# Kernel tuning notes

Measured on AMD Instinct MI355X. Metric: run time of the kernel, lower is better.

The kernel has to match this reference:

```python
import jax, jax.numpy as jnp
import numpy as np

N = 100000
E = 1600000
H = 128
M = 256
L = 6
G = 512          # number of graphs in the batch
A = 95           # num_atom_types
EXTRA = 3        # input_dim - 1
EPS = 1e-5


def swish(x):
    return x * jax.nn.sigmoid(x)


def setup_inputs() -> dict:
    key = jax.random.key(0)
    ks = jax.random.split(key, 16)
    z = jax.random.randint(ks[0], (N, 1), 0, A).astype(jnp.float32)
    extra = jax.random.normal(ks[1], (N, EXTRA), dtype=jnp.float32)
    x = jnp.concatenate([z, extra], axis=1)                     # [N, 4]
    edge_index = jax.random.randint(ks[2], (2, E), 0, N)        # [2, E]
    batch = jnp.sort(jax.random.randint(ks[3], (N,), 0, G))     # [N]
    s = 0.02
    z_embed = jax.random.normal(ks[4], (A, H), dtype=jnp.float32) * s
    extra_w = jax.random.normal(ks[5], (H, EXTRA), dtype=jnp.float32) * (1.0 / np.sqrt(EXTRA))
    extra_b = jnp.zeros((H,), jnp.float32)
    conv_w = jax.random.normal(ks[6], (L, H, H), dtype=jnp.float32) * (1.0 / np.sqrt(H))
    conv_b = jnp.zeros((L, H), jnp.float32)
    gamma = jnp.ones((L, H), jnp.float32)
    beta = jnp.zeros((L, H), jnp.float32)
    mean_scale = jnp.ones((L, H), jnp.float32)
    mlp_w1 = jax.random.normal(ks[7], (L, M, H), dtype=jnp.float32) * (1.0 / np.sqrt(H))
    mlp_b1 = jnp.zeros((L, M), jnp.float32)
    mlp_w2 = jax.random.normal(ks[8], (L, H, M), dtype=jnp.float32) * (1.0 / np.sqrt(M))
    mlp_b2 = jnp.zeros((L, H), jnp.float32)
    return dict(x=x, edge_index=edge_index, batch=batch, z_embed=z_embed,
                extra_w=extra_w, extra_b=extra_b, conv_w=conv_w, conv_b=conv_b,
                gamma=gamma, beta=beta, mean_scale=mean_scale,
                mlp_w1=mlp_w1, mlp_b1=mlp_b1, mlp_w2=mlp_w2, mlp_b2=mlp_b2)


def gnn_forward(x, edge_index, batch, z_embed, extra_w, extra_b, conv_w, conv_b,
                gamma, beta, mean_scale, mlp_w1, mlp_b1, mlp_w2, mlp_b2):
    z = x[:, 0].astype(jnp.int32)
    h = z_embed[z] + x[:, 1:] @ extra_w.T + extra_b                 # [N, H]

    # GCN: add self loops, symmetric normalization (computed once; graph is static)
    loop = jnp.arange(N)
    src = jnp.concatenate([edge_index[0], loop])
    dst = jnp.concatenate([edge_index[1], loop])
    deg = jax.ops.segment_sum(jnp.ones_like(dst, jnp.float32), dst, num_segments=N)
    dinv = jnp.where(deg > 0, jax.lax.rsqrt(jnp.maximum(deg, 1.0)), 0.0)
    norm = (dinv[src] * dinv[dst])[:, None]                         # [E+N, 1]

    cnt = jax.ops.segment_sum(jnp.ones((N,), jnp.float32), batch, num_segments=G)[:, None]
    cnt = jnp.maximum(cnt, 1.0)

    for i in range(L):
        h_res = h
        # GCNConv
        xw = h @ conv_w[i].T
        agg = jax.ops.segment_sum(xw[src] * norm, dst, num_segments=N) + conv_b[i]
        # GraphNorm: gamma * (x - alpha*mean) / sqrt(var + eps) + beta, per graph
        mean = jax.ops.segment_sum(agg, batch, num_segments=G) / cnt   # [G, H]
        sub = agg - mean_scale[i] * mean[batch]
        var = jax.ops.segment_sum(sub * sub, batch, num_segments=G) / cnt
        hn = gamma[i] * sub * jax.lax.rsqrt(var[batch] + EPS) + beta[i]
        ha = swish(hn)
        # residual MLP
        h = swish(swish(ha @ mlp_w1[i].T + mlp_b1[i]) @ mlp_w2[i].T + mlp_b2[i]) + h_res
    return h


def reference(x, edge_index, batch, z_embed, extra_w, extra_b, conv_w, conv_b,
              gamma, beta, mean_scale, mlp_w1, mlp_b1, mlp_w2, mlp_b2):
    return gnn_forward(x, edge_index, batch, z_embed, extra_w, extra_b, conv_w, conv_b,
                       gamma, beta, mean_scale, mlp_w1, mlp_b1, mlp_w2, mlp_b2)
```

## Files before the change

kernel.cpp:

```cpp
#include <hip/hip_runtime.h>

#define NN 100000
#define EE 1600000
#define HH 128
#define MM 256
#define LL 6
#define GG 512
#define SCAN_NB ((NN + 1023) / 1024)

typedef __attribute__((ext_vector_type(8))) short short8;
typedef __attribute__((ext_vector_type(4))) float floatx4;

__device__ __forceinline__ float swishf(float v) {
    return v / (1.0f + __expf(-v));
}

__device__ __forceinline__ unsigned short f2bf(float f) {
    unsigned u = __builtin_bit_cast(unsigned, f);
    unsigned r = u + 0x7FFFu + ((u >> 16) & 1u);
    return (unsigned short)(r >> 16);
}

__device__ __forceinline__ float bf2f(unsigned short u) {
    return __builtin_bit_cast(float, (unsigned)u << 16);
}

__device__ __forceinline__ float2 bf2f2(unsigned u) {
    float2 r;
    r.x = __builtin_bit_cast(float, u << 16);
    r.y = __builtin_bit_cast(float, u & 0xFFFF0000u);
    return r;
}

__device__ __forceinline__ void unpack8(uint4 v, float* a) {
    float2 p0 = bf2f2(v.x), p1 = bf2f2(v.y), p2 = bf2f2(v.z), p3 = bf2f2(v.w);
    a[0] = p0.x; a[1] = p0.y; a[2] = p1.x; a[3] = p1.y;
    a[4] = p2.x; a[5] = p2.y; a[6] = p3.x; a[7] = p3.y;
}

__device__ __forceinline__ uint4 pack8(const float* o) {
    uint4 pk;
    pk.x = (unsigned)f2bf(o[0]) | ((unsigned)f2bf(o[1]) << 16);
    pk.y = (unsigned)f2bf(o[2]) | ((unsigned)f2bf(o[3]) << 16);
    pk.z = (unsigned)f2bf(o[4]) | ((unsigned)f2bf(o[5]) << 16);
    pk.w = (unsigned)f2bf(o[6]) | ((unsigned)f2bf(o[7]) << 16);
    return pk;
}

__device__ __forceinline__ uint2 pack4(const float* o) {
    uint2 pk;
    pk.x = (unsigned)f2bf(o[0]) | ((unsigned)f2bf(o[1]) << 16);
    pk.y = (unsigned)f2bf(o[2]) | ((unsigned)f2bf(o[3]) << 16);
    return pk;
}

__global__ void k_embed(const float* __restrict__ x, const float* __restrict__ z_embed,
                        const float* __restrict__ ew, const float* __restrict__ eb,
                        unsigned short* __restrict__ hb) {
    int idx = blockIdx.x * blockDim.x + threadIdx.x;
    if (idx >= NN * 32) return;
    int n = idx >> 5;
    int c0 = (idx & 31) << 2;
    const float* xr = x + (size_t)n * 4;
    int z = (int)xr[0];
    float x1 = xr[1], x2 = xr[2], x3 = xr[3];
    const float* ze = z_embed + (size_t)z * HH + c0;
    float o[4];
#pragma unroll
    for (int j = 0; j < 4; ++j) {
        int c = c0 + j;
        o[j] = ze[j] + x1 * ew[c * 3 + 0] + x2 * ew[c * 3 + 1] + x3 * ew[c * 3 + 2] + eb[c];
    }
    *(uint2*)(hb + (size_t)n * HH + c0) = pack4(o);
}

__global__ void k_f2bf3(const float* __restrict__ s1, unsigned short* __restrict__ d1, int n1,
                        const float* __restrict__ s2, unsigned short* __restrict__ d2, int n2,
                        const float* __restrict__ s3, unsigned short* __restrict__ d3, int n3) {
    int i = blockIdx.x * blockDim.x + threadIdx.x;
    if (i < n1) {
        d1[i] = f2bf(s1[i]);
    } else if (i < n1 + n2) {
        d2[i - n1] = f2bf(s2[i - n1]);
    } else if (i < n1 + n2 + n3) {
        d3[i - n1 - n2] = f2bf(s3[i - n1 - n2]);
    }
}

__global__ __launch_bounds__(256) void k_degree_p(const int* __restrict__ dst,
                                                  int* __restrict__ deg) {
    int part = blockIdx.x & 7;
    int blk = blockIdx.x >> 3;
    int nb = gridDim.x >> 3;
    int lo = (int)((long long)part * NN / 8);
    int hi = (int)((long long)(part + 1) * NN / 8);
    for (int e = blk * 256 + threadIdx.x; e < EE; e += nb * 256) {
        int d = dst[e];
        if (d >= lo && d < hi) atomicAdd(&deg[d], 1);
    }
}

__global__ void k_dinv(const int* __restrict__ deg, float* __restrict__ dinv) {
    int n = blockIdx.x * blockDim.x + threadIdx.x;
    if (n < NN) dinv[n] = rsqrtf((float)(deg[n] + 1));
}

__global__ void k_scan1(const int* __restrict__ deg, int* __restrict__ bsum) {
    __shared__ int sd[256];
    int t = threadIdx.x;
    int base = blockIdx.x * 1024 + t * 4;
    int s = 0;
#pragma unroll
    for (int j = 0; j < 4; ++j) {
        int i = base + j;
        if (i < NN) s += deg[i];
    }
    sd[t] = s;
    __syncthreads();
    for (int off = 128; off > 0; off >>= 1) {
        if (t < off) sd[t] += sd[t + off];
        __syncthreads();
    }
    if (t == 0) bsum[blockIdx.x] = sd[0];
}

__global__ void k_scan2(const int* __restrict__ bsum, int* __restrict__ boff) {
    __shared__ int sd[128];
    int t = threadIdx.x;
    int v = (t < SCAN_NB) ? bsum[t] : 0;
    sd[t] = v;
    __syncthreads();
    for (int off = 1; off < 128; off <<= 1) {
        int u = (t >= off) ? sd[t - off] : 0;
        __syncthreads();
        sd[t] += u;
        __syncthreads();
    }
    boff[t] = sd[t] - v;
}

__global__ void k_scan3(const int* __restrict__ deg, const int* __restrict__ boff,
                        int* __restrict__ rowptr) {
    __shared__ int sd[256];
    int t = threadIdx.x;
    int base = blockIdx.x * 1024 + t * 4;
    int v[4];
    int s = 0;
#pragma unroll
    for (int j = 0; j < 4; ++j) {
        int i = base + j;
        v[j] = (i < NN) ? deg[i] : 0;
        s += v[j];
    }
    sd[t] = s;
    __syncthreads();
    for (int off = 1; off < 256; off <<= 1) {
        int u = (t >= off) ? sd[t - off] : 0;
        __syncthreads();
        sd[t] += u;
        __syncthreads();
    }
    int run = boff[blockIdx.x] + sd[t] - s;
#pragma unroll
    for (int j = 0; j < 4; ++j) {
        int i = base + j;
        if (i < NN) rowptr[i] = run;
        if (i == NN - 1) rowptr[NN] = run + v[j];
        run += v[j];
    }
}

__global__ __launch_bounds__(256) void k_fill_p(const int* __restrict__ ei,
                                                const int* __restrict__ rowptr,
                                                int* __restrict__ cursor,
                                                int* __restrict__ col) {
    int part = blockIdx.x & 7;
    int blk = blockIdx.x >> 3;
    int nb = gridDim.x >> 3;
    int lo = (int)((long long)part * NN / 8);
    int hi = (int)((long long)(part + 1) * NN / 8);
    for (int e = blk * 256 + threadIdx.x; e < EE; e += nb * 256) {
        int d = ei[EE + e];
        if (d >= lo && d < hi) {
            int p = atomicAdd(&cursor[d], 1);
            col[rowptr[d] + p] = ei[e];
        }
    }
}

__global__ void k_gptr(const int* __restrict__ batch, int* __restrict__ gptr) {
    int n = blockIdx.x * blockDim.x + threadIdx.x;
    if (n >= NN) return;
    int b = batch[n];
    int pb = (n == 0) ? -1 : batch[n - 1];
    for (int g = pb + 1; g <= b; ++g) gptr[g] = n;
    if (n == NN - 1) {
        for (int g = b + 1; g <= GG; ++g) gptr[g] = NN;
    }
}

__global__ __launch_bounds__(256) void k_conv(const unsigned short* __restrict__ A,
                                              const unsigned short* __restrict__ B,
                                              const float* __restrict__ dinv,
                                              unsigned short* __restrict__ Cb) {
    __shared__ unsigned short Bs[128][HH + 8];
    const int tid = threadIdx.x;
    const int wave = tid >> 6;
    const int lane = tid & 63;
    const int quad = lane >> 4;
    const int l16 = lane & 15;
    const int wr = (wave & 1) << 6;
    const int wc = (wave >> 1) << 6;
    const int rowBase = blockIdx.x * 128;

    for (int i = tid; i < 128 * (HH / 8); i += 256) {
        int r = i / (HH / 8);
        int kk = (i % (HH / 8)) * 8;
        int rho = (r & 64) | ((r & 3) << 4) | ((r >> 2) & 15);
        *(uint4*)(&Bs[rho][kk]) = *(const uint4*)(B + (size_t)r * HH + kk);
    }

    floatx4 acc[4][4];
    const floatx4 zed = {0.f, 0.f, 0.f, 0.f};
#pragma unroll
    for (int i = 0; i < 4; ++i)
#pragma unroll
        for (int j = 0; j < 4; ++j) acc[i][j] = zed;

    int ar[4];
#pragma unroll
    for (int i = 0; i < 4; ++i) {
        int r = rowBase + wr + (i << 4) + l16;
        ar[i] = r < NN ? r : NN - 1;
    }

    __syncthreads();

#pragma unroll
    for (int ks = 0; ks < HH / 32; ++ks) {
        int k = (ks << 5) + (quad << 3);
        short8 a[4], b[4];
#pragma unroll
        for (int i = 0; i < 4; ++i) a[i] = *(const short8*)(A + (size_t)ar[i] * HH + k);
#pragma unroll
        for (int j = 0; j < 4; ++j) b[j] = *(const short8*)(&Bs[wc + (j << 4) + l16][k]);
#pragma unroll
        for (int i = 0; i < 4; ++i)
#pragma unroll
            for (int j = 0; j < 4; ++j)
                acc[i][j] =
                    __builtin_amdgcn_mfma_f32_16x16x32_bf16(a[i], b[j], acc[i][j], 0, 0, 0);
    }

    const int c0 = wc + (l16 << 2);
#pragma unroll
    for (int i = 0; i < 4; ++i) {
        int rb = rowBase + wr + (i << 4) + (quad << 2);
#pragma unroll
        for (int reg = 0; reg < 4; ++reg) {
            int r = rb + reg;
            if (r < NN) {
                float dv = dinv[r];
                float o[4];
#pragma unroll
                for (int j = 0; j < 4; ++j) o[j] = acc[i][j][reg] * dv;
                *(uint2*)(Cb + (size_t)r * HH + c0) = pack4(o);
            }
        }
    }
}

__global__ __launch_bounds__(256) void k_agg(const unsigned short* __restrict__ y,
                                             const int* __restrict__ rowptr,
                                             const int* __restrict__ col,
                                             const float* __restrict__ dinv,
                                             const float* __restrict__ cb,
                                             unsigned short* __restrict__ agg) {
    int w = threadIdx.x >> 6;
    int lane = threadIdx.x & 63;
    int d = blockIdx.x * 4 + w;
    if (d >= NN) return;
    int grp = lane >> 4;
    int l16 = lane & 15;
    const uint4* yv = (const uint4*)y;
    float acc[8];
#pragma unroll
    for (int j = 0; j < 8; ++j) acc[j] = 0.f;
    if (grp == 0) {
        uint4 v = yv[(size_t)d * 16 + l16];
        unpack8(v, acc);
    }
    int beg = rowptr[d];
    int end = rowptr[d + 1];
    for (int e = beg + grp; e < end; e += 4) {
        int s = col[e];
        uint4 v = yv[(size_t)s * 16 + l16];
        float b0[8];
        unpack8(v, b0);
#pragma unroll
        for (int k = 0; k < 8; ++k) acc[k] += b0[k];
    }
#pragma unroll
    for (int j = 0; j < 8; ++j) {
        acc[j] += __shfl_xor(acc[j], 16, 64);
        acc[j] += __shfl_xor(acc[j], 32, 64);
    }
    if (grp == 0) {
        float dv = dinv[d];
        float4 c0 = *(const float4*)(cb + l16 * 8);
        float4 c1 = *(const float4*)(cb + l16 * 8 + 4);
        float o[8];
        o[0] = acc[0] * dv + c0.x; o[1] = acc[1] * dv + c0.y;
        o[2] = acc[2] * dv + c0.z; o[3] = acc[3] * dv + c0.w;
        o[4] = acc[4] * dv + c1.x; o[5] = acc[5] * dv + c1.y;
        o[6] = acc[6] * dv + c1.z; o[7] = acc[7] * dv + c1.w;
        *(uint4*)(agg + (size_t)d * HH + l16 * 8) = pack8(o);
    }
}

__global__ __launch_bounds__(512) void k_stats(const unsigned short* __restrict__ agg,
                                               const int* __restrict__ gptr,
                                               const float* __restrict__ ms,
                                               const float* __restrict__ gamma,
                                               const float* __restrict__ beta,
                                               float* __restrict__ c1,
                                               float* __restrict__ c0) {
    __shared__ float s1[512];
    __shared__ float s2[512];
    int g = blockIdx.x;
    int t = threadIdx.x;
    int c = t & 127;
    int part = t >> 7;
    int beg = gptr[g];
    int end = gptr[g + 1];
    float S1 = 0.f, S2 = 0.f;
    for (int n = beg + part; n < end; n += 4) {
        float v = bf2f(agg[(size_t)n * HH + c]);
        S1 += v;
        S2 += v * v;
    }
    s1[t] = S1;
    s2[t] = S2;
    __syncthreads();
    if (part == 0) {
        S1 = (s1[c] + s1[c + 128]) + (s1[c + 256] + s1[c + 384]);
        S2 = (s2[c] + s2[c + 128]) + (s2[c + 256] + s2[c + 384]);
        int cnt = end - beg;
        float inv = 1.0f / (float)(cnt > 0 ? cnt : 1);
        float m = S1 * inv;
        float msc = ms[c];
        float var = S2 * inv - msc * (2.0f - msc) * m * m;
        float rstd = rsqrtf(var + 1e-5f);
        float c1v = gamma[c] * rstd;
        c1[g * HH + c] = c1v;
        c0[g * HH + c] = beta[c] - c1v * msc * m;
    }
}

__global__ __launch_bounds__(256) void k_mega(const unsigned short* __restrict__ agg,
                                              const int* __restrict__ batch,
                                              const float* __restrict__ c1,
                                              const float* __restrict__ c0,
                                              const unsigned short* __restrict__ W1,
                                              const float* __restrict__ b1,
                                              const unsigned short* __restrict__ W2,
                                              const float* __restrict__ b2,
                                              const unsigned short* __restrict__ Wc,
                                              const float* __restrict__ dinv,
                                              unsigned short* __restrict__ hb,
                                              float* __restrict__ h_out,
                                              unsigned short* __restrict__ y_out, int writeF,
                                              int doConv) {
    __shared__ unsigned short ha_s[64 * 136];
    __shared__ unsigned short ts[64 * 264];
    const int tid = threadIdx.x;
    const int wave = tid >> 6;
    const int lane = tid & 63;
    const int quad = lane >> 4;
    const int l16 = lane & 15;
    const int rowBase = blockIdx.x * 64;
    const floatx4 zed = {0.f, 0.f, 0.f, 0.f};

    {
        int lr = tid >> 2;
        int coff = (tid & 3) << 5;
        int r = rowBase + lr;
        if (r >= NN) r = NN - 1;
        int g = batch[r];
        const float* c1p = c1 + g * HH + coff;
        const float* c0p = c0 + g * HH + coff;
#pragma unroll
        for (int q = 0; q < 4; ++q) {
            uint4 raw = *(const uint4*)(agg + (size_t)r * HH + coff + (q << 3));
            float v[8];
            unpack8(raw, v);
            float4 ca = *(const float4*)(c1p + (q << 3));
            float4 cb4 = *(const float4*)(c1p + (q << 3) + 4);
            float4 da = *(const float4*)(c0p + (q << 3));
            float4 db = *(const float4*)(c0p + (q << 3) + 4);
            float cc1[8] = {ca.x, ca.y, ca.z, ca.w, cb4.x, cb4.y, cb4.z, cb4.w};
            float cc0[8] = {da.x, da.y, da.z, da.w, db.x, db.y, db.z, db.w};
            float o[8];
#pragma unroll
            for (int j = 0; j < 8; ++j) o[j] = swishf(cc1[j] * v[j] + cc0[j]);
            *(uint4*)(&ha_s[lr * 136 + coff + (q << 3)]) = pack8(o);
        }
    }
    __syncthreads();

    {
        const int wca = wave << 6;
        floatx4 acc1[4][4];
#pragma unroll
        for (int i = 0; i < 4; ++i)
#pragma unroll
            for (int j = 0; j < 4; ++j) acc1[i][j] = zed;
#pragma unroll
        for (int ks = 0; ks < 4; ++ks) {
            int k = (ks << 5) + (quad << 3);
            short8 a[4], b[4];
#pragma unroll
            for (int i = 0; i < 4; ++i)
                a[i] = *(const short8*)(&ha_s[((i << 4) + l16) * 136 + k]);
#pragma unroll
            for (int j = 0; j < 4; ++j)
                b[j] = *(const short8*)(W1 + (size_t)(wca + (l16 << 2) + j) * HH + k);
#pragma unroll
            for (int i = 0; i < 4; ++i)
#pragma unroll
                for (int j = 0; j < 4; ++j)
                    acc1[i][j] =
                        __builtin_amdgcn_mfma_f32_16x16x32_bf16(a[i], b[j], acc1[i][j], 0, 0, 0);
        }
        const int ct = wca + (l16 << 2);
        float4 b4 = *(const float4*)(b1 + ct);
        float bv[4] = {b4.x, b4.y, b4.z, b4.w};
#pragma unroll
        for (int i = 0; i < 4; ++i) {
#pragma unroll
            for (int reg = 0; reg < 4; ++reg) {
                int lr = (i << 4) + (quad << 2) + reg;
                float o[4];
#pragma unroll
                for (int j = 0; j < 4; ++j) o[j] = swishf(acc1[i][j][reg] + bv[j]);
                *(uint2*)(&ts[lr * 264 + ct]) = pack4(o);
            }
        }
    }
    __syncthreads();

    const int wrb = (wave & 1) << 5;
    const int wcb = (wave >> 1) << 6;
    const int co = wcb + (l16 << 2);
    {
        floatx4 acc2[2][4];
#pragma unroll
        for (int i = 0; i < 2; ++i)
#pragma unroll
            for (int j = 0; j < 4; ++j) acc2[i][j] = zed;
#pragma unroll
        for (int ks = 0; ks < 8; ++ks) {
            int k = (ks << 5) + (quad << 3);
            short8 a[2], b[4];
#pragma unroll
            for (int i = 0; i < 2; ++i)
                a[i] = *(const short8*)(&ts[(wrb + (i << 4) + l16) * 264 + k]);
#pragma unroll
            for (int j = 0; j < 4; ++j)
                b[j] = *(const short8*)(W2 + (size_t)(wcb + (l16 << 2) + j) * MM + k);
#pragma unroll
            for (int i = 0; i < 2; ++i)
#pragma unroll
                for (int j = 0; j < 4; ++j)
                    acc2[i][j] =
                        __builtin_amdgcn_mfma_f32_16x16x32_bf16(a[i], b[j], acc2[i][j], 0, 0, 0);
        }
        float4 b4 = *(const float4*)(b2 + co);
        float bv[4] = {b4.x, b4.y, b4.z, b4.w};
#pragma unroll
        for (int i = 0; i < 2; ++i) {
#pragma unroll
            for (int reg = 0; reg < 4; ++reg) {
                int lr = wrb + (i << 4) + (quad << 2) + reg;
                int r = rowBase + lr;
                if (r < NN) {
                    uint2 rv = *(const uint2*)(hb + (size_t)r * HH + co);
                    float2 r01 = bf2f2(rv.x), r23 = bf2f2(rv.y);
                    float o[4];
                    o[0] = swishf(acc2[i][0][reg] + bv[0]) + r01.x;
                    o[1] = swishf(acc2[i][1][reg] + bv[1]) + r01.y;
                    o[2] = swishf(acc2[i][2][reg] + bv[2]) + r23.x;
                    o[3] = swishf(acc2[i][3][reg] + bv[3]) + r23.y;
                    uint2 pk = pack4(o);
                    *(uint2*)(hb + (size_t)r * HH + co) = pk;
                    if (writeF)
                        *(float4*)(h_out + (size_t)r * HH + co) =
                            make_float4(o[0], o[1], o[2], o[3]);
                    *(uint2*)(&ha_s[lr * 136 + co]) = pk;
                } else {
                    *(uint2*)(&ha_s[lr * 136 + co]) = make_uint2(0u, 0u);
                }
            }
        }
    }

    if (doConv) {
        __syncthreads();
        floatx4 acc3[2][4];
#pragma unroll
        for (int i = 0; i < 2; ++i)
#pragma unroll
            for (int j = 0; j < 4; ++j) acc3[i][j] = zed;
#pragma unroll
        for (int ks = 0; ks < 4; ++ks) {
            int k = (ks << 5) + (quad << 3);
            short8 a[2], b[4];
#pragma unroll
            for (int i = 0; i < 2; ++i)
                a[i] = *(const short8*)(&ha_s[(wrb + (i << 4) + l16) * 136 + k]);
#pragma unroll
            for (int j = 0; j < 4; ++j)
                b[j] = *(const short8*)(Wc + (size_t)(wcb + (l16 << 2) + j) * HH + k);
#pragma unroll
            for (int i = 0; i < 2; ++i)
#pragma unroll
                for (int j = 0; j < 4; ++j)
                    acc3[i][j] =
                        __builtin_amdgcn_mfma_f32_16x16x32_bf16(a[i], b[j], acc3[i][j], 0, 0, 0);
        }
#pragma unroll
        for (int i = 0; i < 2; ++i) {
#pragma unroll
            for (int reg = 0; reg < 4; ++reg) {
                int r = rowBase + wrb + (i << 4) + (quad << 2) + reg;
                if (r < NN) {
                    float dv = dinv[r];
                    float o[4];
#pragma unroll
                    for (int j = 0; j < 4; ++j) o[j] = acc3[i][j][reg] * dv;
                    *(uint2*)(y_out + (size_t)r * HH + co) = pack4(o);
                }
            }
        }
    }
}

extern "C" void kernel_launch(void* const* d_in, const int* in_sizes, int n_in,
                              void* d_out, int out_size, void* d_ws, size_t ws_size,
                              hipStream_t stream) {
    const float* x = (const float*)d_in[0];
    const int* ei = (const int*)d_in[1];
    const int* batch = (const int*)d_in[2];
    const float* z_embed = (const float*)d_in[3];
    const float* extra_w = (const float*)d_in[4];
    const float* extra_b = (const float*)d_in[5];
    const float* conv_w = (const float*)d_in[6];
    const float* conv_b = (const float*)d_in[7];
    const float* gamma = (const float*)d_in[8];
    const float* beta = (const float*)d_in[9];
    const float* mean_scale = (const float*)d_in[10];
    const float* mlp_w1 = (const float*)d_in[11];
    const float* mlp_b1 = (const float*)d_in[12];
    const float* mlp_w2 = (const float*)d_in[13];
    const float* mlp_b2 = (const float*)d_in[14];
    float* h_out = (float*)d_out;

    char* wsB = (char*)d_ws;
    size_t off = 0;
    auto alloc = [&](size_t bytes) -> void* {
        void* p = (void*)(wsB + off);
        off = (off + bytes + 255) & ~(size_t)255;
        return p;
    };
    float* dinv = (float*)alloc((size_t)NN * 4);
    int* deg = (int*)alloc((size_t)NN * 4);
    int* cursor = (int*)alloc((size_t)NN * 4);
    int* rowptr = (int*)alloc((size_t)(NN + 1) * 4);
    int* bsum = (int*)alloc(128 * 4);
    int* boff = (int*)alloc(128 * 4);
    int* col = (int*)alloc((size_t)EE * 4);
    int* gptr = (int*)alloc((size_t)(GG + 1) * 4);
    float* c1t = (float*)alloc((size_t)GG * HH * 4);
    float* c0t = (float*)alloc((size_t)GG * HH * 4);
    unsigned short* wb =
        (unsigned short*)alloc((size_t)(LL * (HH * HH + MM * HH + HH * MM)) * 2);
    unsigned short* cwb = wb;
    unsigned short* w1b = wb + (size_t)LL * HH * HH;
    unsigned short* w2b = w1b + (size_t)LL * MM * HH;
    unsigned short* hb = (unsigned short*)alloc((size_t)NN * HH * 2);
    unsigned short* ybuf = (unsigned short*)alloc((size_t)NN * HH * 2);
    unsigned short* aggb = (unsigned short*)alloc((size_t)NN * HH * 2);

    hipMemsetAsync(deg, 0, (size_t)NN * 4, stream);
    hipMemsetAsync(cursor, 0, (size_t)NN * 4, stream);

    k_embed<<<(NN * 32 + 255) / 256, 256, 0, stream>>>(x, z_embed, extra_w, extra_b, hb);
    {
        int n1 = LL * HH * HH, n2 = LL * MM * HH, n3 = LL * HH * MM;
        int nt = n1 + n2 + n3;
        k_f2bf3<<<(nt + 255) / 256, 256, 0, stream>>>(conv_w, cwb, n1, mlp_w1, w1b, n2,
                                                      mlp_w2, w2b, n3);
    }
    k_degree_p<<<1024, 256, 0, stream>>>(ei + EE, deg);
    k_dinv<<<(NN + 255) / 256, 256, 0, stream>>>(deg, dinv);
    k_scan1<<<SCAN_NB, 256, 0, stream>>>(deg, bsum);
    k_scan2<<<1, 128, 0, stream>>>(bsum, boff);
    k_scan3<<<SCAN_NB, 256, 0, stream>>>(deg, boff, rowptr);
    k_fill_p<<<1024, 256, 0, stream>>>(ei, rowptr, cursor, col);
    k_gptr<<<(NN + 255) / 256, 256, 0, stream>>>(batch, gptr);

    int gconv = (NN + 127) / 128;
    int gmega = (NN + 63) / 64;
    k_conv<<<gconv, 256, 0, stream>>>(hb, cwb, dinv, ybuf);
    for (int i = 0; i < LL; ++i) {
        k_agg<<<(NN + 3) / 4, 256, 0, stream>>>(ybuf, rowptr, col, dinv,
                                                conv_b + (size_t)i * HH, aggb);
        k_stats<<<GG, 512, 0, stream>>>(aggb, gptr, mean_scale + (size_t)i * HH,
                                        gamma + (size_t)i * HH, beta + (size_t)i * HH, c1t,
                                        c0t);
        k_mega<<<gmega, 256, 0, stream>>>(
            aggb, batch, c1t, c0t, w1b + (size_t)i * MM * HH, mlp_b1 + (size_t)i * MM,
            w2b + (size_t)i * HH * MM, mlp_b2 + (size_t)i * HH,
            cwb + (size_t)(i + 1 < LL ? i + 1 : 0) * HH * HH, dinv, hb, h_out, ybuf,
            i == LL - 1 ? 1 : 0, i < LL - 1 ? 1 : 0);
    }
}
```

Before: 1.346 ms.

## Fuse per-graph GraphNorm statistics into aggregation kernel via atomics

The aggregation kernel now also accumulates per-graph sum and sum-of-squares. It reduces the four rows handled by a block in shared memory and adds them to global buffers with atomics, which removes the separate k_stats pass that re-read the whole agg tensor. A small finalize kernel then turns the sums into the scale and shift coefficients and zeroes the accumulators for the next layer. In exchange it adds a block-wide sync and many float atomics per block, and summation order becomes nondeterministic. k_mega also gains a launch-bounds occupancy hint of 3.

New measurement: 1.334 ms. About the same (-0.9%).

```diff
diff --git a/kernel.cpp b/kernel.cpp
--- a/kernel.cpp
+++ b/kernel.cpp
@@ -275,23 +275,32 @@
                                              const int* __restrict__ col,
                                              const float* __restrict__ dinv,
                                              const float* __restrict__ cb,
-                                             unsigned short* __restrict__ agg) {
+                                             const int* __restrict__ batch,
+                                             unsigned short* __restrict__ agg,
+                                             float* __restrict__ S1g,
+                                             float* __restrict__ S2g) {
+    __shared__ float s1s[4][128];
+    __shared__ float s2s[4][128];
+    __shared__ int sg[4];
     int w = threadIdx.x >> 6;
     int lane = threadIdx.x & 63;
     int d = blockIdx.x * 4 + w;
-    if (d >= NN) return;
+    bool valid = d < NN;
     int grp = lane >> 4;
     int l16 = lane & 15;
     const uint4* yv = (const uint4*)y;
     float acc[8];
 #pragma unroll
     for (int j = 0; j < 8; ++j) acc[j] = 0.f;
-    if (grp == 0) {
+    if (grp == 0 && valid) {
         uint4 v = yv[(size_t)d * 16 + l16];
         unpack8(v, acc);
     }
-    int beg = rowptr[d];
-    int end = rowptr[d + 1];
+    int beg = 0, end = 0;
+    if (valid) {
+        beg = rowptr[d];
+        end = rowptr[d + 1];
+    }
     for (int e = beg + grp; e < end; e += 4) {
         int s = col[e];
         uint4 v = yv[(size_t)s * 16 + l16];
@@ -306,71 +315,100 @@
         acc[j] += __shfl_xor(acc[j], 32, 64);
     }
     if (grp == 0) {
-        float dv = dinv[d];
-        float4 c0 = *(const float4*)(cb + l16 * 8);
-        float4 c1 = *(const float4*)(cb + l16 * 8 + 4);
-        float o[8];
-        o[0] = acc[0] * dv + c0.x; o[1] = acc[1] * dv + c0.y;
-        o[2] = acc[2] * dv + c0.z; o[3] = acc[3] * dv + c0.w;
-        o[4] = acc[4] * dv + c1.x; o[5] = acc[5] * dv + c1.y;
-        o[6] = acc[6] * dv + c1.z; o[7] = acc[7] * dv + c1.w;
-        *(uint4*)(agg + (size_t)d * HH + l16 * 8) = pack8(o);
-    }
-}
-
-__global__ __launch_bounds__(512) void k_stats(const unsigned short* __restrict__ agg,
-                                               const int* __restrict__ gptr,
-                                               const float* __restrict__ ms,
-                                               const float* __restrict__ gamma,
-                                               const float* __restrict__ beta,
-                                               float* __restrict__ c1,
-                                               float* __restrict__ c0) {
-    __shared__ float s1[512];
-    __shared__ float s2[512];
+        if (valid) {
+            float dv = dinv[d];
+            float4 c0 = *(const float4*)(cb + l16 * 8);
+            float4 c1 = *(const float4*)(cb + l16 * 8 + 4);
+            float o[8];
+            o[0] = acc[0] * dv + c0.x; o[1] = acc[1] * dv + c0.y;
+            o[2] = acc[2] * dv + c0.z; o[3] = acc[3] * dv + c0.w;
+            o[4] = acc[4] * dv + c1.x; o[5] = acc[5] * dv + c1.y;
+            o[6] = acc[6] * dv + c1.z; o[7] = acc[7] * dv + c1.w;
+            unsigned short us[8];
+#pragma unroll
+            for (int j = 0; j < 8; ++j) us[j] = f2bf(o[j]);
+            uint4 pk;
+            pk.x = (unsigned)us[0] | ((unsigned)us[1] << 16);
+            pk.y = (unsigned)us[2] | ((unsigned)us[3] << 16);
+            pk.z = (unsigned)us[4] | ((unsigned)us[5] << 16);
+            pk.w = (unsigned)us[6] | ((unsigned)us[7] << 16);
+            *(uint4*)(agg + (size_t)d * HH + l16 * 8) = pk;
+#pragma unroll
+            for (int j = 0; j < 8; ++j) {
+                float orv = bf2f(us[j]);
+                s1s[w][l16 * 8 + j] = orv;
+                s2s[w][l16 * 8 + j] = orv * orv;
+            }
+        } else {
+#pragma unroll
+            for (int j = 0; j < 8; ++j) {
+                s1s[w][l16 * 8 + j] = 0.f;
+                s2s[w][l16 * 8 + j] = 0.f;
+            }
+        }
+        if (l16 == 0) sg[w] = valid ? batch[d] : -1;
+    }
+    __syncthreads();
+    if (threadIdx.x < 128) {
+        int c = threadIdx.x;
+        int g0 = sg[0], g1 = sg[1], g2 = sg[2], g3 = sg[3];
+        if (g0 >= 0 && g0 == g1 && g0 == g2 && g0 == g3) {
+            float a = (s1s[0][c] + s1s[1][c]) + (s1s[2][c] + s1s[3][c]);
+            float b = (s2s[0][c] + s2s[1][c]) + (s2s[2][c] + s2s[3][c]);
+            atomicAdd(&S1g[g0 * HH + c], a);
+            atomicAdd(&S2g[g0 * HH + c], b);
+        } else {
+            int gs[4] = {g0, g1, g2, g3};
+#pragma unroll
+            for (int ww = 0; ww < 4; ++ww) {
+                if (gs[ww] >= 0) {
+                    atomicAdd(&S1g[gs[ww] * HH + c], s1s[ww][c]);
+                    atomicAdd(&S2g[gs[ww] * HH + c], s2s[ww][c]);
+                }
+            }
+        }
+    }
+}
+
+__global__ __launch_bounds__(128) void k_finalize(const int* __restrict__ gptr,
+                                                  const float* __restrict__ ms,
+                                                  const float* __restrict__ gamma,
+                                                  const float* __restrict__ beta,
+                                                  float* __restrict__ S1g,
+                                                  float* __restrict__ S2g,
+                                                  float* __restrict__ c1,
+                                                  float* __restrict__ c0) {
     int g = blockIdx.x;
-    int t = threadIdx.x;
-    int c = t & 127;
-    int part = t >> 7;
-    int beg = gptr[g];
-    int end = gptr[g + 1];
-    float S1 = 0.f, S2 = 0.f;
-    for (int n = beg + part; n < end; n += 4) {
-        float v = bf2f(agg[(size_t)n * HH + c]);
-        S1 += v;
-        S2 += v * v;
-    }
-    s1[t] = S1;
-    s2[t] = S2;
-    __syncthreads();
-    if (part == 0) {
-        S1 = (s1[c] + s1[c + 128]) + (s1[c + 256] + s1[c + 384]);
-        S2 = (s2[c] + s2[c + 128]) + (s2[c + 256] + s2[c + 384]);
-        int cnt = end - beg;
-        float inv = 1.0f / (float)(cnt > 0 ? cnt : 1);
-        float m = S1 * inv;
-        float msc = ms[c];
-        float var = S2 * inv - msc * (2.0f - msc) * m * m;
-        float rstd = rsqrtf(var + 1e-5f);
-        float c1v = gamma[c] * rstd;
-        c1[g * HH + c] = c1v;
-        c0[g * HH + c] = beta[c] - c1v * msc * m;
-    }
-}
-
-__global__ __launch_bounds__(256) void k_mega(const unsigned short* __restrict__ agg,
-                                              const int* __restrict__ batch,
-                                              const float* __restrict__ c1,
-                                              const float* __restrict__ c0,
-                                              const unsigned short* __restrict__ W1,
-                                              const float* __restrict__ b1,
-                                              const unsigned short* __restrict__ W2,
-                                              const float* __restrict__ b2,
-                                              const unsigned short* __restrict__ Wc,
-                                              const float* __restrict__ dinv,
-                                              unsigned short* __restrict__ hb,
-                                              float* __restrict__ h_out,
-                                              unsigned short* __restrict__ y_out, int writeF,
-                                              int doConv) {
+    int c = threadIdx.x;
+    int cnt = gptr[g + 1] - gptr[g];
+    float inv = 1.0f / (float)(cnt > 0 ? cnt : 1);
+    float S1 = S1g[g * HH + c];
+    float S2 = S2g[g * HH + c];
+    float m = S1 * inv;
+    float msc = ms[c];
+    float var = S2 * inv - msc * (2.0f - msc) * m * m;
+    float rstd = rsqrtf(var + 1e-5f);
+    float c1v = gamma[c] * rstd;
+    c1[g * HH + c] = c1v;
+    c0[g * HH + c] = beta[c] - c1v * msc * m;
+    S1g[g * HH + c] = 0.f;
+    S2g[g * HH + c] = 0.f;
+}
+
+__global__ __launch_bounds__(256, 3) void k_mega(const unsigned short* __restrict__ agg,
+                                                 const int* __restrict__ batch,
+                                                 const float* __restrict__ c1,
+                                                 const float* __restrict__ c0,
+                                                 const unsigned short* __restrict__ W1,
+                                                 const float* __restrict__ b1,
+                                                 const unsigned short* __restrict__ W2,
+                                                 const float* __restrict__ b2,
+                                                 const unsigned short* __restrict__ Wc,
+                                                 const float* __restrict__ dinv,
+                                                 unsigned short* __restrict__ hb,
+                                                 float* __restrict__ h_out,
+                                                 unsigned short* __restrict__ y_out,
+                                                 int writeF, int doConv) {
     __shared__ unsigned short ha_s[64 * 136];
     __shared__ unsigned short ts[64 * 264];
     const int tid = threadIdx.x;
@@ -582,6 +620,8 @@
     int* gptr = (int*)alloc((size_t)(GG + 1) * 4);
     float* c1t = (float*)alloc((size_t)GG * HH * 4);
     float* c0t = (float*)alloc((size_t)GG * HH * 4);
+    float* S1g = (float*)alloc((size_t)GG * HH * 4);
+    float* S2g = (float*)alloc((size_t)GG * HH * 4);
     unsigned short* wb =
         (unsigned short*)alloc((size_t)(LL * (HH * HH + MM * HH + HH * MM)) * 2);
     unsigned short* cwb = wb;
@@ -593,6 +633,8 @@
 
     hipMemsetAsync(deg, 0, (size_t)NN * 4, stream);
     hipMemsetAsync(cursor, 0, (size_t)NN * 4, stream);
+    hipMemsetAsync(S1g, 0, (size_t)GG * HH * 4, stream);
+    hipMemsetAsync(S2g, 0, (size_t)GG * HH * 4, stream);
 
     k_embed<<<(NN * 32 + 255) / 256, 256, 0, stream>>>(x, z_embed, extra_w, extra_b, hb);
     {
@@ -614,10 +656,11 @@
     k_conv<<<gconv, 256, 0, stream>>>(hb, cwb, dinv, ybuf);
     for (int i = 0; i < LL; ++i) {
         k_agg<<<(NN + 3) / 4, 256, 0, stream>>>(ybuf, rowptr, col, dinv,
-                                                conv_b + (size_t)i * HH, aggb);
-        k_stats<<<GG, 512, 0, stream>>>(aggb, gptr, mean_scale + (size_t)i * HH,
-                                        gamma + (size_t)i * HH, beta + (size_t)i * HH, c1t,
-                                        c0t);
+                                                conv_b + (size_t)i * HH, batch, aggb, S1g,
+                                                S2g);
+        k_finalize<<<GG, 128, 0, stream>>>(gptr, mean_scale + (size_t)i * HH,
+                                           gamma + (size_t)i * HH, beta + (size_t)i * HH,
+                                           S1g, S2g, c1t, c0t);
         k_mega<<<gmega, 256, 0, stream>>>(
             aggb, batch, c1t, c0t, w1b + (size_t)i * MM * HH, mlp_b1 + (size_t)i * MM,
             w2b + (size_t)i * HH * MM, mlp_b2 + (size_t)i * HH,
```
